# Optimization experiments

Measured on AMD Instinct MI355X. Metric: run time of the kernel, lower is better.

Reference implementation:

```python
import jax, jax.numpy as jnp
import numpy as np

BIAS_BASE = 1.0
HEADS = 8
TOPK = 32
NEG_INF = -1e30


def setup_inputs() -> dict:
    key = jax.random.key(0)
    ks = jax.random.split(key, 7)
    B, N, T, D = 8, 256, 128, 256
    s = 1.0 / np.sqrt(D)
    return {
        'h_val': jax.random.normal(ks[0], (B, N, T, D), jnp.float32),
        'z_map': jax.random.normal(ks[1], (B, N, D), jnp.float32),
        'base_adj': jax.random.uniform(ks[2], (B, N, N), jnp.float32),
        'Wq': jax.random.normal(ks[3], (D, D), jnp.float32) * s,
        'Wk': jax.random.normal(ks[4], (D, D), jnp.float32) * s,
        'Wv': jax.random.normal(ks[5], (D, D), jnp.float32) * s,
        'Wo': jax.random.normal(ks[6], (D, D), jnp.float32) * s,
    }


def reference(h_val, z_map, base_adj, Wq, Wk, Wv, Wo):
    B, N, T, D = h_val.shape
    H = HEADS
    hd = D // H
    scale = 1.0 / np.sqrt(hd)

    # q, k: [B, H, N, hd] (Linear with no bias: x @ W.T)
    q = (z_map @ Wq.T).reshape(B, N, H, hd).transpose(0, 2, 1, 3)
    k = (z_map @ Wk.T).reshape(B, N, H, hd).transpose(0, 2, 1, 3)

    scores = jnp.einsum('bhid,bhjd->bhij', q, k) * scale
    # log-adjacency bias, broadcast over heads
    bias = jnp.log(jnp.clip(base_adj, 1e-12, None))
    scores = scores + BIAS_BASE * bias[:, None, :, :]

    raw_attn = jax.nn.softmax(scores, axis=-1)

    # top-k mask: keep entries >= k-th largest per row (ties measure-zero for
    # continuous scores; matches torch.topk scatter mask)
    kth = jax.lax.top_k(scores, TOPK)[0][..., -1:]
    masked = jnp.where(scores >= kth, scores, NEG_INF)
    attn = jax.nn.softmax(masked, axis=-1)

    # v: [B, H, N, T, hd]
    v = (h_val @ Wv.T).reshape(B, N, T, H, hd).transpose(0, 3, 1, 2, 4)
    mixed = jnp.einsum('bhij,bhjtd->bhitd', attn, v)
    mixed = mixed.transpose(0, 2, 3, 1, 4).reshape(B, N, T, D)
    mixed = mixed @ Wo.T

    out = h_val + mixed  # dropout is identity in eval / p=0
    return out, attn.mean(axis=1), raw_attn.mean(axis=1)
```

## Files before the change

### kernel.cpp

```cpp
#include <hip/hip_runtime.h>
#include <stdint.h>

#define BB 8
#define NN 256
#define TT 128
#define DD 256
#define HH 8
#define HD 32
#define KTOP 32

typedef short bf16x8 __attribute__((ext_vector_type(8)));
typedef float f32x4 __attribute__((ext_vector_type(4)));

static __device__ __forceinline__ short f2bf(float f) {
  uint32_t u = __float_as_uint(f);
  u += 0x7FFFu + ((u >> 16) & 1u);
  return (short)(u >> 16);
}

static __device__ __forceinline__ uint32_t skey(float f) {
  uint32_t u = __float_as_uint(f);
  return (u & 0x80000000u) ? ~u : (u | 0x80000000u);
}

static __device__ __forceinline__ f32x4 mfma16(bf16x8 a, bf16x8 b, f32x4 c) {
  return __builtin_amdgcn_mfma_f32_16x16x32_bf16(a, b, c, 0, 0, 0);
}

__global__ __launch_bounds__(256) void k_cvt(const float* __restrict__ wv,
                                             const float* __restrict__ wo,
                                             short* __restrict__ wvb,
                                             short* __restrict__ wob) {
  int idx = blockIdx.x * 256 + threadIdx.x;
  wvb[idx] = f2bf(wv[idx]);
  wob[idx] = f2bf(wo[idx]);
}

__global__ __launch_bounds__(256) void k_qk(const float* __restrict__ z,
                                            const float* __restrict__ Wq,
                                            const float* __restrict__ Wk,
                                            float* __restrict__ q,
                                            float* __restrict__ kk) {
  int b = blockIdx.x >> 4;
  int i0 = (blockIdx.x & 15) * 16;
  __shared__ float zl[DD][16];
  int tid = threadIdx.x;
  for (int r = 0; r < 16; ++r)
    zl[tid][r] = z[(size_t)(b * NN + i0 + r) * DD + tid];
  __syncthreads();
  float aq[16], ak[16];
#pragma unroll
  for (int r = 0; r < 16; ++r) { aq[r] = 0.f; ak[r] = 0.f; }
  int o = tid;
  const float4* zc = reinterpret_cast<const float4*>(&zl[0][0]);
  for (int kx = 0; kx < DD; ++kx) {
    float wq = Wq[(size_t)o * DD + kx];
    float wk = Wk[(size_t)o * DD + kx];
    float zr[16];
    ((float4*)zr)[0] = zc[kx * 4 + 0];
    ((float4*)zr)[1] = zc[kx * 4 + 1];
    ((float4*)zr)[2] = zc[kx * 4 + 2];
    ((float4*)zr)[3] = zc[kx * 4 + 3];
#pragma unroll
    for (int r = 0; r < 16; ++r) {
      aq[r] = fmaf(zr[r], wq, aq[r]);
      ak[r] = fmaf(zr[r], wk, ak[r]);
    }
  }
  for (int r = 0; r < 16; ++r) {
    q[(size_t)(b * NN + i0 + r) * DD + o] = aq[r];
    kk[(size_t)(b * NN + i0 + r) * DD + o] = ak[r];
  }
}

__global__ __launch_bounds__(256) void k_attn(const float* __restrict__ q,
                                              const float* __restrict__ kmat,
                                              const float* __restrict__ adj,
                                              short* __restrict__ attn,
                                              float* __restrict__ attn_mean,
                                              float* __restrict__ raw_mean) {
  int b = blockIdx.x >> 8;
  int i = blockIdx.x & 255;
  __shared__ float ql[DD];
  __shared__ float bias[NN];
  __shared__ float sc[HH][NN];
  __shared__ float ms[HH], invraw[HH], invs2[HH];
  __shared__ uint32_t thr[HH];
  int tid = threadIdx.x;
  ql[tid] = q[(size_t)(b * NN + i) * DD + tid];
  bias[tid] = logf(fmaxf(adj[(size_t)(b * NN + i) * NN + tid], 1e-12f));
  __syncthreads();
  int wv = tid >> 6, lane = tid & 63;
  const float scale = 0.17677669529663687f;
  for (int hh = 0; hh < 2; ++hh) {
    int h = wv * 2 + hh;
    float sv[4];
#pragma unroll
    for (int c = 0; c < 4; ++c) {
      int j = lane + 64 * c;
      const float4* kp =
          (const float4*)&kmat[(size_t)(b * NN + j) * DD + h * HD];
      float s = 0.f;
#pragma unroll
      for (int d4 = 0; d4 < 8; ++d4) {
        float4 kv = kp[d4];
        s = fmaf(ql[h * HD + d4 * 4 + 0], kv.x, s);
        s = fmaf(ql[h * HD + d4 * 4 + 1], kv.y, s);
        s = fmaf(ql[h * HD + d4 * 4 + 2], kv.z, s);
        s = fmaf(ql[h * HD + d4 * 4 + 3], kv.w, s);
      }
      sv[c] = s * scale + bias[j];
      sc[h][j] = sv[c];
    }
    float m = fmaxf(fmaxf(sv[0], sv[1]), fmaxf(sv[2], sv[3]));
    for (int off = 32; off > 0; off >>= 1) m = fmaxf(m, __shfl_xor(m, off, 64));
    float e = expf(sv[0] - m) + expf(sv[1] - m) + expf(sv[2] - m) +
              expf(sv[3] - m);
    for (int off = 32; off > 0; off >>= 1) e += __shfl_xor(e, off, 64);
    uint32_t kb[4];
#pragma unroll
    for (int c = 0; c < 4; ++c) kb[c] = skey(sv[c]);
    uint32_t lo = 0u, hi = 0xFFFFFFFFu;
    for (int it = 0; it < 32; ++it) {
      uint32_t mid = (uint32_t)(((uint64_t)lo + (uint64_t)hi + 1ull) >> 1);
      int cnt = 0;
#pragma unroll
      for (int c = 0; c < 4; ++c)
        cnt += __popcll(__ballot(kb[c] >= mid));
      if (cnt >= KTOP) lo = mid; else hi = mid - 1u;
    }
    float e2 = 0.f;
#pragma unroll
    for (int c = 0; c < 4; ++c)
      e2 += (kb[c] >= lo) ? expf(sv[c] - m) : 0.f;
    for (int off = 32; off > 0; off >>= 1) e2 += __shfl_xor(e2, off, 64);
    if (lane == 0) {
      ms[h] = m; invraw[h] = 1.f / e; invs2[h] = 1.f / e2; thr[h] = lo;
    }
  }
  __syncthreads();
  int j = tid;
  float rm = 0.f, am = 0.f;
#pragma unroll
  for (int h = 0; h < HH; ++h) {
    float s = sc[h][j];
    float e = expf(s - ms[h]);
    rm += e * invraw[h];
    float a = (skey(s) >= thr[h]) ? e * invs2[h] : 0.f;
    am += a;
    attn[((size_t)(b * HH + h) * NN + i) * NN + j] = f2bf(a);
  }
  raw_mean[(size_t)(b * NN + i) * NN + j] = rm * 0.125f;
  attn_mean[(size_t)(b * NN + i) * NN + j] = am * 0.125f;
}

__global__ __launch_bounds__(256) void k_vproj(const float* __restrict__ hv,
                                               const short* __restrict__ wvb,
                                               short* __restrict__ vws) {
  int bid = blockIdx.x;
  int jb = bid & 3;
  int t = (bid >> 2) & (TT - 1);
  int b = bid >> 9;
  int j0 = jb * 64;
  __shared__ short wl[256 * 40];
  int tid = threadIdx.x, wv = tid >> 6, lane = tid & 63;
  int lrow = lane & 15, quad = lane >> 4;
  f32x4 acc[16];
#pragma unroll
  for (int m = 0; m < 16; ++m) acc[m] = (f32x4){0.f, 0.f, 0.f, 0.f};
  int j = j0 + wv * 16 + lrow;
  const float* hrow = &hv[((size_t)(b * NN + j) * TT + t) * DD];
  for (int kc = 0; kc < 8; ++kc) {
    __syncthreads();
    {
      const int4* src = (const int4*)&wvb[(size_t)tid * DD + kc * 32];
      int4* dst = (int4*)&wl[tid * 40];
      dst[0] = src[0]; dst[1] = src[1]; dst[2] = src[2]; dst[3] = src[3];
    }
    __syncthreads();
    const float4* hp = (const float4*)&hrow[kc * 32 + quad * 8];
    float4 f0 = hp[0], f1 = hp[1];
    bf16x8 bfrag;
    bfrag[0] = f2bf(f0.x); bfrag[1] = f2bf(f0.y);
    bfrag[2] = f2bf(f0.z); bfrag[3] = f2bf(f0.w);
    bfrag[4] = f2bf(f1.x); bfrag[5] = f2bf(f1.y);
    bfrag[6] = f2bf(f1.z); bfrag[7] = f2bf(f1.w);
#pragma unroll
    for (int mt = 0; mt < 16; ++mt) {
      const bf16x8* ap = (const bf16x8*)&wl[(mt * 16 + lrow) * 40 + quad * 8];
      acc[mt] = mfma16(*ap, bfrag, acc[mt]);
    }
  }
#pragma unroll
  for (int mt = 0; mt < 16; ++mt) {
#pragma unroll
    for (int r = 0; r < 4; ++r) {
      int o = mt * 16 + quad * 4 + r;
      int h = o >> 5, dp = o & 31;
      vws[(((size_t)(b * HH + h) * TT + t) * HD + dp) * NN + j] =
          f2bf(acc[mt][r]);
    }
  }
}

__global__ __launch_bounds__(256) void k_mix(const short* __restrict__ attn,
                                             const short* __restrict__ vws,
                                             short* __restrict__ mixed) {
  int bid = blockIdx.x;
  int ct = bid & 15;
  int it = (bid >> 4) & 1;
  int bh = bid >> 5;
  int b = bh >> 3, h = bh & 7;
  int i0 = it * 128, c0 = ct * 256;
  __shared__ short vl[256 * 40];
  int tid = threadIdx.x, wv = tid >> 6, lane = tid & 63;
  int lrow = lane & 15, quad = lane >> 4;
  f32x4 acc[2][16];
#pragma unroll
  for (int mi = 0; mi < 2; ++mi)
#pragma unroll
    for (int nt = 0; nt < 16; ++nt) acc[mi][nt] = (f32x4){0.f, 0.f, 0.f, 0.f};
  const short* abase = &attn[((size_t)bh * NN + i0) * NN];
  const short* vbase = &vws[(size_t)bh * 4096 * NN + (size_t)c0 * NN];
  for (int kc = 0; kc < 8; ++kc) {
    __syncthreads();
    {
      const int4* src = (const int4*)&vbase[(size_t)tid * NN + kc * 32];
      int4* dst = (int4*)&vl[tid * 40];
      dst[0] = src[0]; dst[1] = src[1]; dst[2] = src[2]; dst[3] = src[3];
    }
    __syncthreads();
    bf16x8 afrag[2];
#pragma unroll
    for (int mi = 0; mi < 2; ++mi)
      afrag[mi] = *(const bf16x8*)&abase[(size_t)((wv * 2 + mi) * 16 + lrow) *
                                             NN + kc * 32 + quad * 8];
#pragma unroll
    for (int nt = 0; nt < 16; ++nt) {
      bf16x8 bfrag = *(const bf16x8*)&vl[(nt * 16 + lrow) * 40 + quad * 8];
      acc[0][nt] = mfma16(afrag[0], bfrag, acc[0][nt]);
      acc[1][nt] = mfma16(afrag[1], bfrag, acc[1][nt]);
    }
  }
#pragma unroll
  for (int mi = 0; mi < 2; ++mi)
#pragma unroll
    for (int nt = 0; nt < 16; ++nt)
#pragma unroll
      for (int r = 0; r < 4; ++r) {
        int i = i0 + (wv * 2 + mi) * 16 + quad * 4 + r;
        int col = c0 + nt * 16 + lrow;
        int t = col >> 5, dp = col & 31;
        mixed[((size_t)(b * NN + i) * TT + t) * DD + h * HD + dp] =
            f2bf(acc[mi][nt][r]);
      }
}

__global__ __launch_bounds__(256, 2) void k_out(const short* __restrict__ mixed,
                                                const short* __restrict__ wob,
                                                const float* __restrict__ hv,
                                                float* __restrict__ out) {
  __shared__ short wl[128 * 256];
  int tid = threadIdx.x;
  int half = blockIdx.x & 1;
  size_t row0 = (size_t)(blockIdx.x >> 1) * 128;
  int wv = tid >> 6, lane = tid & 63;
  int lrow = lane & 15, quad = lane >> 4;

  bf16x8 afrag[2][8];
  {
    const short* a0 = &mixed[(row0 + wv * 32 + lrow) * DD];
    const short* a1 = &mixed[(row0 + wv * 32 + 16 + lrow) * DD];
#pragma unroll
    for (int kc = 0; kc < 8; ++kc) {
      afrag[0][kc] = *(const bf16x8*)&a0[kc * 32 + quad * 8];
      afrag[1][kc] = *(const bf16x8*)&a1[kc * 32 + quad * 8];
    }
  }
  {
    int row = tid >> 1, seg = tid & 1;
    const int4* src =
        (const int4*)&wob[(size_t)(half * 128 + row) * DD + seg * 128];
#pragma unroll
    for (int g = 0; g < 16; ++g) {
      int gg = seg * 16 + g;
      int dstb = row * 512 + ((gg * 16) ^ ((row & 7) << 4));
      *(int4*)((char*)wl + dstb) = src[g];
    }
  }
  __syncthreads();

  f32x4 acc[2][8];
#pragma unroll
  for (int mi = 0; mi < 2; ++mi)
#pragma unroll
    for (int nt = 0; nt < 8; ++nt) acc[mi][nt] = (f32x4){0.f, 0.f, 0.f, 0.f};
#pragma unroll
  for (int kc = 0; kc < 8; ++kc) {
#pragma unroll
    for (int nt = 0; nt < 8; ++nt) {
      int brow = nt * 16 + lrow;
      int boff = brow * 512 + ((kc * 64 + quad * 16) ^ ((brow & 7) << 4));
      bf16x8 bfrag = *(const bf16x8*)((const char*)wl + boff);
      acc[0][nt] = mfma16(afrag[0][kc], bfrag, acc[0][nt]);
      acc[1][nt] = mfma16(afrag[1][kc], bfrag, acc[1][nt]);
    }
  }
  __syncthreads();

#pragma unroll
  for (int mi = 0; mi < 2; ++mi)
#pragma unroll
    for (int r = 0; r < 4; ++r) {
      size_t row = row0 + wv * 32 + mi * 16 + quad * 4 + r;
#pragma unroll
      for (int nt = 0; nt < 8; ++nt) {
        int o = half * 128 + nt * 16 + lrow;
        out[row * DD + o] = acc[mi][nt][r] + hv[row * DD + o];
      }
    }
}

extern "C" void kernel_launch(void* const* d_in, const int* in_sizes, int n_in,
                              void* d_out, int out_size, void* d_ws,
                              size_t ws_size, hipStream_t stream) {
  (void)in_sizes; (void)n_in; (void)out_size; (void)ws_size;
  const float* hv  = (const float*)d_in[0];
  const float* z   = (const float*)d_in[1];
  const float* adj = (const float*)d_in[2];
  const float* Wq  = (const float*)d_in[3];
  const float* Wk  = (const float*)d_in[4];
  const float* Wv  = (const float*)d_in[5];
  const float* Wo  = (const float*)d_in[6];
  float* out = (float*)d_out;
  float* attn_mean = out + (size_t)BB * NN * TT * DD;
  float* raw_mean = attn_mean + (size_t)BB * NN * NN;

  char* ws = (char*)d_ws;
  float* q = (float*)ws;      ws += (size_t)BB * NN * DD * 4;
  float* k = (float*)ws;      ws += (size_t)BB * NN * DD * 4;
  short* wvb = (short*)ws;    ws += (size_t)DD * DD * 2;
  short* wob = (short*)ws;    ws += (size_t)DD * DD * 2;
  short* attn = (short*)ws;   ws += (size_t)BB * HH * NN * NN * 2;
  short* vws = (short*)ws;    ws += (size_t)BB * HH * TT * HD * NN * 2;
  short* mixed = (short*)ws;  ws += (size_t)BB * NN * TT * DD * 2;

  hipLaunchKernelGGL(k_cvt, dim3(DD * DD / 256), dim3(256), 0, stream,
                     Wv, Wo, wvb, wob);
  hipLaunchKernelGGL(k_qk, dim3(BB * 16), dim3(256), 0, stream,
                     z, Wq, Wk, q, k);
  hipLaunchKernelGGL(k_attn, dim3(BB * NN), dim3(256), 0, stream,
                     q, k, adj, attn, attn_mean, raw_mean);
  hipLaunchKernelGGL(k_vproj, dim3(BB * TT * 4), dim3(256), 0, stream,
                     hv, wvb, vws);
  hipLaunchKernelGGL(k_mix, dim3(BB * HH * 2 * 16), dim3(256), 0, stream,
                     attn, vws, mixed);
  hipLaunchKernelGGL(k_out, dim3((BB * NN * TT / 128) * 2), dim3(256), 0,
                     stream, mixed, wob, hv, out);
}
```

Before: 931.5 us.

## Restructure V-projection to keep half of Wv resident in LDS across time steps

The V-projection kernel now loads a 128-row half of the bf16 Wv into a swizzled LDS tile once per block and reuses it across 8 time steps and 128 node rows. Previously every block reloaded the full weight in small chunks. hv fp32 loads are double-buffered in registers, prefetched two k-chunks ahead, including across time-step boundaries. The grid shrinks to 512 blocks with larger per-block work and launch bounds asking for 2 blocks per CU, which raises register pressure and LDS use (64KB per block) and may lower occupancy.

```diff
diff --git a/kernel.cpp b/kernel.cpp
--- a/kernel.cpp
+++ b/kernel.cpp
@@ -154,52 +154,99 @@
   attn_mean[(size_t)(b * NN + i) * NN + j] = am * 0.125f;
 }
 
-__global__ __launch_bounds__(256) void k_vproj(const float* __restrict__ hv,
-                                               const short* __restrict__ wvb,
-                                               short* __restrict__ vws) {
+__global__ __launch_bounds__(256, 2) void k_vproj(const float* __restrict__ hv,
+                                                  const short* __restrict__ wvb,
+                                                  short* __restrict__ vws) {
+  __shared__ short wl[128 * 256];
   int bid = blockIdx.x;
-  int jb = bid & 3;
-  int t = (bid >> 2) & (TT - 1);
-  int b = bid >> 9;
-  int j0 = jb * 64;
-  __shared__ short wl[256 * 40];
+  int b = bid & 7;
+  int half_o = (bid >> 3) & 1;
+  int half_j = (bid >> 4) & 1;
+  int tg = bid >> 5;
+  int t0 = tg * 8;
   int tid = threadIdx.x, wv = tid >> 6, lane = tid & 63;
   int lrow = lane & 15, quad = lane >> 4;
-  f32x4 acc[16];
-#pragma unroll
-  for (int m = 0; m < 16; ++m) acc[m] = (f32x4){0.f, 0.f, 0.f, 0.f};
-  int j = j0 + wv * 16 + lrow;
-  const float* hrow = &hv[((size_t)(b * NN + j) * TT + t) * DD];
-  for (int kc = 0; kc < 8; ++kc) {
-    __syncthreads();
-    {
-      const int4* src = (const int4*)&wvb[(size_t)tid * DD + kc * 32];
-      int4* dst = (int4*)&wl[tid * 40];
-      dst[0] = src[0]; dst[1] = src[1]; dst[2] = src[2]; dst[3] = src[3];
-    }
-    __syncthreads();
-    const float4* hp = (const float4*)&hrow[kc * 32 + quad * 8];
-    float4 f0 = hp[0], f1 = hp[1];
-    bf16x8 bfrag;
-    bfrag[0] = f2bf(f0.x); bfrag[1] = f2bf(f0.y);
-    bfrag[2] = f2bf(f0.z); bfrag[3] = f2bf(f0.w);
-    bfrag[4] = f2bf(f1.x); bfrag[5] = f2bf(f1.y);
-    bfrag[6] = f2bf(f1.z); bfrag[7] = f2bf(f1.w);
-#pragma unroll
-    for (int mt = 0; mt < 16; ++mt) {
-      const bf16x8* ap = (const bf16x8*)&wl[(mt * 16 + lrow) * 40 + quad * 8];
-      acc[mt] = mfma16(*ap, bfrag, acc[mt]);
-    }
-  }
-#pragma unroll
-  for (int mt = 0; mt < 16; ++mt) {
-#pragma unroll
-    for (int r = 0; r < 4; ++r) {
-      int o = mt * 16 + quad * 4 + r;
-      int h = o >> 5, dp = o & 31;
-      vws[(((size_t)(b * HH + h) * TT + t) * HD + dp) * NN + j] =
-          f2bf(acc[mt][r]);
-    }
+  int j0 = half_j * 128 + wv * 32;
+
+  const float* p0 = &hv[((size_t)(b * NN + j0 + lrow) * TT + t0) * DD];
+  const float* p1 = &hv[((size_t)(b * NN + j0 + 16 + lrow) * TT + t0) * DD];
+
+  float4 st[2][4];
+  st[0][0] = *(const float4*)(p0 + 0 * 32 + quad * 8);
+  st[0][1] = *(const float4*)(p0 + 0 * 32 + quad * 8 + 4);
+  st[0][2] = *(const float4*)(p1 + 0 * 32 + quad * 8);
+  st[0][3] = *(const float4*)(p1 + 0 * 32 + quad * 8 + 4);
+  st[1][0] = *(const float4*)(p0 + 1 * 32 + quad * 8);
+  st[1][1] = *(const float4*)(p0 + 1 * 32 + quad * 8 + 4);
+  st[1][2] = *(const float4*)(p1 + 1 * 32 + quad * 8);
+  st[1][3] = *(const float4*)(p1 + 1 * 32 + quad * 8 + 4);
+
+  {
+    int row = tid >> 1, seg = tid & 1;
+    const int4* src =
+        (const int4*)&wvb[(size_t)(half_o * 128 + row) * DD + seg * 128];
+#pragma unroll
+    for (int g = 0; g < 16; ++g) {
+      int gg = seg * 16 + g;
+      int dstb = row * 512 + ((gg * 16) ^ ((row & 7) << 4));
+      *(int4*)((char*)wl + dstb) = src[g];
+    }
+  }
+  __syncthreads();
+
+  for (int tt = 0; tt < 8; ++tt) {
+    int t = t0 + tt;
+    const float* p0n = (tt == 7) ? p0 : p0 + DD;
+    const float* p1n = (tt == 7) ? p1 : p1 + DD;
+    f32x4 acc[2][8];
+#pragma unroll
+    for (int nt = 0; nt < 2; ++nt)
+#pragma unroll
+      for (int mt = 0; mt < 8; ++mt) acc[nt][mt] = (f32x4){0.f, 0.f, 0.f, 0.f};
+#pragma unroll
+    for (int kc = 0; kc < 8; ++kc) {
+      const int cur = kc & 1;
+      bf16x8 bf0, bf1;
+      bf0[0] = f2bf(st[cur][0].x); bf0[1] = f2bf(st[cur][0].y);
+      bf0[2] = f2bf(st[cur][0].z); bf0[3] = f2bf(st[cur][0].w);
+      bf0[4] = f2bf(st[cur][1].x); bf0[5] = f2bf(st[cur][1].y);
+      bf0[6] = f2bf(st[cur][1].z); bf0[7] = f2bf(st[cur][1].w);
+      bf1[0] = f2bf(st[cur][2].x); bf1[1] = f2bf(st[cur][2].y);
+      bf1[2] = f2bf(st[cur][2].z); bf1[3] = f2bf(st[cur][2].w);
+      bf1[4] = f2bf(st[cur][3].x); bf1[5] = f2bf(st[cur][3].y);
+      bf1[6] = f2bf(st[cur][3].z); bf1[7] = f2bf(st[cur][3].w);
+      if (kc < 6) {
+        st[cur][0] = *(const float4*)(p0 + (kc + 2) * 32 + quad * 8);
+        st[cur][1] = *(const float4*)(p0 + (kc + 2) * 32 + quad * 8 + 4);
+        st[cur][2] = *(const float4*)(p1 + (kc + 2) * 32 + quad * 8);
+        st[cur][3] = *(const float4*)(p1 + (kc + 2) * 32 + quad * 8 + 4);
+      } else {
+        st[cur][0] = *(const float4*)(p0n + (kc - 6) * 32 + quad * 8);
+        st[cur][1] = *(const float4*)(p0n + (kc - 6) * 32 + quad * 8 + 4);
+        st[cur][2] = *(const float4*)(p1n + (kc - 6) * 32 + quad * 8);
+        st[cur][3] = *(const float4*)(p1n + (kc - 6) * 32 + quad * 8 + 4);
+      }
+#pragma unroll
+      for (int mt = 0; mt < 8; ++mt) {
+        int brow = mt * 16 + lrow;
+        int boff = brow * 512 + ((kc * 64 + quad * 16) ^ ((brow & 7) << 4));
+        bf16x8 af = *(const bf16x8*)((const char*)wl + boff);
+        acc[0][mt] = mfma16(af, bf0, acc[0][mt]);
+        acc[1][mt] = mfma16(af, bf1, acc[1][mt]);
+      }
+    }
+#pragma unroll
+    for (int mt = 0; mt < 8; ++mt)
+#pragma unroll
+      for (int r = 0; r < 4; ++r) {
+        int o = half_o * 128 + mt * 16 + quad * 4 + r;
+        int h = o >> 5, dp = o & 31;
+        size_t base = (((size_t)(b * HH + h) * TT + t) * HD + dp) * NN + j0;
+        vws[base + lrow] = f2bf(acc[0][mt][r]);
+        vws[base + 16 + lrow] = f2bf(acc[1][mt][r]);
+      }
+    p0 = p0n;
+    p1 = p1n;
   }
 }
 
@@ -351,7 +398,7 @@
                      z, Wq, Wk, q, k);
   hipLaunchKernelGGL(k_attn, dim3(BB * NN), dim3(256), 0, stream,
                      q, k, adj, attn, attn_mean, raw_mean);
-  hipLaunchKernelGGL(k_vproj, dim3(BB * TT * 4), dim3(256), 0, stream,
+  hipLaunchKernelGGL(k_vproj, dim3(512), dim3(256), 0, stream,
                      hv, wvb, vws);
   hipLaunchKernelGGL(k_mix, dim3(BB * HH * 2 * 16), dim3(256), 0, stream,
                      attn, vws, mixed);
```

After: 1.043 ms. +12.0%, slower.

## Restructure k_mix to stage full-K V tile in swizzled LDS once

Applied to the files above, without the earlier changes.

The attention-times-V mixing kernel now loads a 128-column by 256-K V tile into LDS in a single pass, using an XOR swizzle in place of padding to avoid bank conflicts. Each wave preloads all of its attention A fragments into registers up front. This removes the per-K-chunk sync and reload loop, and the grid grows to twice as many blocks with half the column width each. The cost is 64KB of LDS per block with a launch bound of two blocks per CU, more registers held for A fragments, and no overlap between loads and MFMA inside a block.

```diff
diff --git a/kernel.cpp b/kernel.cpp
--- a/kernel.cpp
+++ b/kernel.cpp
@@ -203,52 +203,67 @@
   }
 }
 
-__global__ __launch_bounds__(256) void k_mix(const short* __restrict__ attn,
-                                             const short* __restrict__ vws,
-                                             short* __restrict__ mixed) {
+__global__ __launch_bounds__(256, 2) void k_mix(const short* __restrict__ attn,
+                                                const short* __restrict__ vws,
+                                                short* __restrict__ mixed) {
+  __shared__ short wl[128 * 256];
   int bid = blockIdx.x;
-  int ct = bid & 15;
-  int it = (bid >> 4) & 1;
-  int bh = bid >> 5;
+  int cb = bid & 31;
+  int ib = (bid >> 5) & 1;
+  int bh = bid >> 6;
   int b = bh >> 3, h = bh & 7;
-  int i0 = it * 128, c0 = ct * 256;
-  __shared__ short vl[256 * 40];
+  int c0 = cb * 128, i0 = ib * 128;
   int tid = threadIdx.x, wv = tid >> 6, lane = tid & 63;
   int lrow = lane & 15, quad = lane >> 4;
-  f32x4 acc[2][16];
+
+  bf16x8 afrag[2][8];
+  {
+    const short* a0 = &attn[((size_t)bh * NN + i0 + wv * 32 + lrow) * NN];
+    const short* a1 = a0 + 16 * NN;
+#pragma unroll
+    for (int kc = 0; kc < 8; ++kc) {
+      afrag[0][kc] = *(const bf16x8*)&a0[kc * 32 + quad * 8];
+      afrag[1][kc] = *(const bf16x8*)&a1[kc * 32 + quad * 8];
+    }
+  }
+  {
+    int row = tid >> 1, seg = tid & 1;
+    const int4* src =
+        (const int4*)&vws[((size_t)bh * 4096 + c0 + row) * NN + seg * 128];
+#pragma unroll
+    for (int g = 0; g < 16; ++g) {
+      int gg = seg * 16 + g;
+      int dstb = row * 512 + ((gg * 16) ^ ((row & 7) << 4));
+      *(int4*)((char*)wl + dstb) = src[g];
+    }
+  }
+  __syncthreads();
+
+  f32x4 acc[2][8];
 #pragma unroll
   for (int mi = 0; mi < 2; ++mi)
 #pragma unroll
-    for (int nt = 0; nt < 16; ++nt) acc[mi][nt] = (f32x4){0.f, 0.f, 0.f, 0.f};
-  const short* abase = &attn[((size_t)bh * NN + i0) * NN];
-  const short* vbase = &vws[(size_t)bh * 4096 * NN + (size_t)c0 * NN];
+    for (int nt = 0; nt < 8; ++nt) acc[mi][nt] = (f32x4){0.f, 0.f, 0.f, 0.f};
+#pragma unroll
   for (int kc = 0; kc < 8; ++kc) {
-    __syncthreads();
-    {
-      const int4* src = (const int4*)&vbase[(size_t)tid * NN + kc * 32];
-      int4* dst = (int4*)&vl[tid * 40];
-      dst[0] = src[0]; dst[1] = src[1]; dst[2] = src[2]; dst[3] = src[3];
-    }
-    __syncthreads();
-    bf16x8 afrag[2];
-#pragma unroll
-    for (int mi = 0; mi < 2; ++mi)
-      afrag[mi] = *(const bf16x8*)&abase[(size_t)((wv * 2 + mi) * 16 + lrow) *
-                                             NN + kc * 32 + quad * 8];
-#pragma unroll
-    for (int nt = 0; nt < 16; ++nt) {
-      bf16x8 bfrag = *(const bf16x8*)&vl[(nt * 16 + lrow) * 40 + quad * 8];
-      acc[0][nt] = mfma16(afrag[0], bfrag, acc[0][nt]);
-      acc[1][nt] = mfma16(afrag[1], bfrag, acc[1][nt]);
-    }
-  }
+#pragma unroll
+    for (int nt = 0; nt < 8; ++nt) {
+      int brow = nt * 16 + lrow;
+      int boff = brow * 512 + ((kc * 64 + quad * 16) ^ ((brow & 7) << 4));
+      bf16x8 bfrag = *(const bf16x8*)((const char*)wl + boff);
+      acc[0][nt] = mfma16(afrag[0][kc], bfrag, acc[0][nt]);
+      acc[1][nt] = mfma16(afrag[1][kc], bfrag, acc[1][nt]);
+    }
+  }
+  __syncthreads();
+
 #pragma unroll
   for (int mi = 0; mi < 2; ++mi)
 #pragma unroll
-    for (int nt = 0; nt < 16; ++nt)
+    for (int nt = 0; nt < 8; ++nt)
 #pragma unroll
       for (int r = 0; r < 4; ++r) {
-        int i = i0 + (wv * 2 + mi) * 16 + quad * 4 + r;
+        int i = i0 + wv * 32 + mi * 16 + quad * 4 + r;
         int col = c0 + nt * 16 + lrow;
         int t = col >> 5, dp = col & 31;
         mixed[((size_t)(b * NN + i) * TT + t) * DD + h * HD + dp] =
@@ -353,7 +368,7 @@
                      q, k, adj, attn, attn_mean, raw_mean);
   hipLaunchKernelGGL(k_vproj, dim3(BB * TT * 4), dim3(256), 0, stream,
                      hv, wvb, vws);
-  hipLaunchKernelGGL(k_mix, dim3(BB * HH * 2 * 16), dim3(256), 0, stream,
+  hipLaunchKernelGGL(k_mix, dim3(64 * 2 * 32), dim3(256), 0, stream,
                      attn, vws, mixed);
   hipLaunchKernelGGL(k_out, dim3((BB * NN * TT / 128) * 2), dim3(256), 0,
                      stream, mixed, wob, hv, out);
```

Result: faster. 891.5 us (-4.3%).
